# Kernel optimization log

Measured on AMD Instinct MI355X. Metric: run time of the kernel, lower is better.

Reference implementation:

```python
import jax, jax.numpy as jnp
import numpy as np

B, N, D, W = 4, 4096, 256, 7
K = 2 * W + 1  # 15 taps: positions [i-2w, ..., i]
H = 4 * D
EPS = 1e-5


def layer_norm(x, g, b):
    mu = jnp.mean(x, axis=-1, keepdims=True)
    var = jnp.mean(jnp.square(x - mu), axis=-1, keepdims=True)
    return (x - mu) * jax.lax.rsqrt(var + EPS) * g + b


def setup_inputs() -> dict:
    key = jax.random.key(0)
    ks = jax.random.split(key, 8)
    s = 0.02
    return {
        "x": jax.random.normal(ks[0], (B, N, D), dtype=jnp.float32),
        # w_mix[k] is the DxD block of the (K*D -> D) Linear acting on offset k-2w
        "w_mix": (jax.random.normal(ks[1], (K, D, D), dtype=jnp.float32) * s),
        "b_mix": jnp.zeros((D,), dtype=jnp.float32),
        "g1": jnp.ones((D,), jnp.float32) + 0.1 * jax.random.normal(ks[2], (D,), jnp.float32),
        "b1": 0.1 * jax.random.normal(ks[3], (D,), jnp.float32),
        "w_ff1": jax.random.normal(ks[4], (D, H), dtype=jnp.float32) * s,
        "b_ff1": jnp.zeros((H,), dtype=jnp.float32),
        "w_ff2": jax.random.normal(ks[5], (H, D), dtype=jnp.float32) * s,
        "b_ff2": jnp.zeros((D,), dtype=jnp.float32),
        "g2": jnp.ones((D,), jnp.float32) + 0.1 * jax.random.normal(ks[6], (D,), jnp.float32),
        "b2": 0.1 * jax.random.normal(ks[7], (D,), jnp.float32),
    }


def reference(x, w_mix, b_mix, g1, b1, w_ff1, b_ff1, w_ff2, b_ff2, g2, b2):
    # Causal windowed concat + Linear == causal 1D conv with kernel K=2w+1.
    # torch feats chunk k holds x[i - 2w + k]; conv tap k with left pad 2w
    # sees exactly x[i - 2w + k], so kernel = mix weight reshaped (K, D, D).
    mix = jax.lax.conv_general_dilated(
        x, w_mix, window_strides=(1,), padding=[(2 * W, 0)],
        dimension_numbers=("NWC", "WIO", "NWC"),
    ) + b_mix  # [B, N, D]
    # Dropout is identity in eval mode (reference baseline).
    h = layer_norm(x + mix, g1, b1)
    ff = jnp.dot(jax.nn.gelu(jnp.dot(h, w_ff1) + b_ff1, approximate=False), w_ff2) + b_ff2
    return layer_norm(h + ff, g2, b2)
```

## Files before the change

kernel.cpp:

```cpp
#include <hip/hip_runtime.h>
#include <cstdint>

#define DD     256
#define HH     1024
#define NNSEQ  4096
#define MT     32
#define XR     46
#define XPITCH 264
#define SLOTP  260
#define EPSLN  1e-5f

typedef unsigned short u16;
typedef __attribute__((ext_vector_type(8))) short short8;
typedef __attribute__((ext_vector_type(4))) float f32x4;

#define MFMA(a, b, c) __builtin_amdgcn_mfma_f32_16x16x32_bf16(a, b, c, 0, 0, 0)

__device__ __forceinline__ u16 f2bf(float f) {
  unsigned u = __float_as_uint(f);
  u += 0x7FFF + ((u >> 16) & 1);
  return (u16)(u >> 16);
}
__device__ __forceinline__ float bf2f(u16 s) { return __uint_as_float(((unsigned)s) << 16); }

__device__ __forceinline__ float fast_gelu(float v) {
  const float e = __expf(v * __builtin_fmaf(v * v, -0.0713548163f, -1.5957691216f));
  return v * __builtin_amdgcn_rcpf(1.f + e);
}

__global__ __launch_bounds__(256) void k_prep(
    const float* __restrict__ wmix, const float* __restrict__ wff1,
    const float* __restrict__ wff2, u16* __restrict__ wpk,
    u16* __restrict__ w1pk, u16* __restrict__ w2pk)
{
  __shared__ float t[32][257];
  const int b = blockIdx.x, tid = threadIdx.x;

  u16* dst;
  if (b < 120) {
    dst = wpk + (size_t)b * 8192;
    for (int r = 0; r < 32; ++r)
      t[r][tid] = wmix[(size_t)(b * 32 + r) * 256 + tid];
  } else if (b < 152) {
    const int u = b - 120, c2 = u >> 3, s = u & 7;
    dst = w1pk + (size_t)u * 8192;
    for (int r = 0; r < 32; ++r)
      t[r][tid] = wff1[(size_t)(s * 32 + r) * 1024 + c2 * 256 + tid];
  } else {
    const int u = b - 152, c2 = u >> 3, s = u & 7;
    dst = w2pk + (size_t)u * 8192;
    for (int r = 0; r < 32; ++r)
      t[r][tid] = wff2[(size_t)(c2 * 256 + s * 32 + r) * 256 + tid];
  }
  __syncthreads();

  const int l = tid & 63, q = l >> 4, cl = l & 15;
#pragma unroll
  for (int f = 0; f < 4; ++f) {
    const int fi = f * 4 + (tid >> 6);
    const int n = fi * 16 + cl;
    uint4 pk;
    unsigned* p = (unsigned*)&pk;
#pragma unroll
    for (int jj = 0; jj < 4; ++jj)
      p[jj] = (unsigned)f2bf(t[q * 8 + jj * 2][n]) | ((unsigned)f2bf(t[q * 8 + jj * 2 + 1][n]) << 16);
    *(uint4*)&dst[(size_t)fi * 512 + l * 8] = pk;
  }
}

__global__ __launch_bounds__(512, 4) void k_fused(
    const float* __restrict__ x, const u16* __restrict__ wpk,
    const float* __restrict__ bmix, const float* __restrict__ g1,
    const float* __restrict__ b1, const u16* __restrict__ w1pk,
    const float* __restrict__ bf1, const u16* __restrict__ w2pk,
    const float* __restrict__ bf2, const float* __restrict__ g2,
    const float* __restrict__ b2, float* __restrict__ out)
{
  __shared__ __align__(16) u16 bufA[XR * XPITCH];
  __shared__ __align__(16) u16 asbuf[2 * MT * XPITCH];
  __shared__ float redS[8][MT], redS2[8][MT];
  __shared__ float muL[MT], invL[MT];

#define bufB ((float*)asbuf)

  const int tid = threadIdx.x;
  const int wv = tid >> 6, l = tid & 63, q = l >> 4, cl = l & 15;
  const int mg = wv >> 2, ng = wv & 3;
  const long tok0 = (long)blockIdx.x * MT;
  const int n0 = (int)(tok0 & (NNSEQ - 1));

  {
    const int cslot = (tid & 63) * 4;
    for (int r = tid >> 6; r < XR; r += 8) {
      const int nloc = n0 - 14 + r;
      float4 v = make_float4(0.f, 0.f, 0.f, 0.f);
      if (nloc >= 0) v = *(const float4*)&x[(tok0 - 14 + r) * DD + cslot];
      uint2 pk;
      pk.x = (unsigned)f2bf(v.x) | ((unsigned)f2bf(v.y) << 16);
      pk.y = (unsigned)f2bf(v.z) | ((unsigned)f2bf(v.w) << 16);
      *(uint2*)&bufA[r * XPITCH + cslot] = pk;
    }
  }
  __syncthreads();

  f32x4 acc[2][4];
#pragma unroll
  for (int nt = 0; nt < 4; ++nt) {
    const float bm = (mg == 0) ? bmix[ng * 64 + nt * 16 + cl] : 0.f;
#pragma unroll
    for (int mt = 0; mt < 2; ++mt) acc[mt][nt] = (f32x4){bm, bm, bm, bm};
  }

  const u16* bbase = wpk + (size_t)(mg * 60) * 8192 + (size_t)(ng * 4) * 512 + (size_t)l * 8;

#define LOAD_A(dst, s_)                                                         \
  {                                                                             \
    const int ks = mg * 60 + (s_);                                              \
    const int xrow = ks >> 3, c0 = (ks & 7) * 32;                               \
    _Pragma("unroll")                                                           \
    for (int mt = 0; mt < 2; ++mt)                                              \
      dst[mt] = *(const short8*)&bufA[(xrow + mt * 16 + cl) * XPITCH + c0 + q * 8]; \
  }
#define LOAD_B(dst, s_)                                                         \
  {                                                                             \
    const u16* bp = bbase + (size_t)(s_) * 8192;                                \
    _Pragma("unroll")                                                           \
    for (int nt = 0; nt < 4; ++nt)                                              \
      dst[nt] = *(const short8*)(bp + nt * 512);                                \
  }

  {
    short8 af[2][2], bfr[2][4];
    LOAD_A(af[0], 0) LOAD_B(bfr[0], 0)
    LOAD_A(af[1], 1) LOAD_B(bfr[1], 1)

#pragma unroll 2
    for (int s = 0; s < 60; ++s) {
      const int cur = s & 1;
#pragma unroll
      for (int mt = 0; mt < 2; ++mt)
#pragma unroll
        for (int nt = 0; nt < 4; ++nt)
          acc[mt][nt] = MFMA(af[cur][mt], bfr[cur][nt], acc[mt][nt]);
      if (s + 2 < 60) {
        LOAD_A(af[cur], s + 2)
        LOAD_B(bfr[cur], s + 2)
      }
    }
  }
#undef LOAD_A
#undef LOAD_B

  if (mg == 1) {
#pragma unroll
    for (int mt = 0; mt < 2; ++mt)
#pragma unroll
      for (int nt = 0; nt < 4; ++nt)
#pragma unroll
        for (int reg = 0; reg < 4; ++reg)
          bufB[(mt * 16 + q * 4 + reg) * SLOTP + ng * 64 + nt * 16 + cl] = acc[mt][nt][reg];
  }
  __syncthreads();

  if (mg == 0) {
    float ps[2][4], ps2[2][4];
#pragma unroll
    for (int mt = 0; mt < 2; ++mt)
#pragma unroll
      for (int reg = 0; reg < 4; ++reg) {
        const int row = mt * 16 + q * 4 + reg;
        float s = 0.f, s2 = 0.f;
#pragma unroll
        for (int nt = 0; nt < 4; ++nt) {
          const int col = ng * 64 + nt * 16 + cl;
          const float y = acc[mt][nt][reg] + bufB[row * SLOTP + col]
                        + x[(tok0 + row) * DD + col];
          acc[mt][nt][reg] = y;
          s += y; s2 += y * y;
        }
#pragma unroll
        for (int off = 1; off < 16; off <<= 1) { s += __shfl_xor(s, off, 64); s2 += __shfl_xor(s2, off, 64); }
        ps[mt][reg] = s; ps2[mt][reg] = s2;
      }
    if (cl == 0) {
#pragma unroll
      for (int mt = 0; mt < 2; ++mt)
#pragma unroll
        for (int reg = 0; reg < 4; ++reg) {
          const int row = mt * 16 + q * 4 + reg;
          redS[ng][row] = ps[mt][reg]; redS2[ng][row] = ps2[mt][reg];
        }
    }
  }
  __syncthreads();
  if (tid < MT) {
    const float s  = redS[0][tid] + redS[1][tid] + redS[2][tid] + redS[3][tid];
    const float s2 = redS2[0][tid] + redS2[1][tid] + redS2[2][tid] + redS2[3][tid];
    const float mu = s * (1.f / DD);
    const float var = s2 * (1.f / DD) - mu * mu;
    muL[tid] = mu; invL[tid] = rsqrtf(var + EPSLN);
  }
  __syncthreads();

  if (mg == 0) {
#pragma unroll
    for (int nt = 0; nt < 4; ++nt) {
      const int col = ng * 64 + nt * 16 + cl;
      const float gv = g1[col], bv = b1[col];
#pragma unroll
      for (int mt = 0; mt < 2; ++mt)
#pragma unroll
        for (int reg = 0; reg < 4; ++reg) {
          const int row = mt * 16 + q * 4 + reg;
          const float hv = (acc[mt][nt][reg] - muL[row]) * invL[row] * gv + bv;
          bufA[row * XPITCH + col] = f2bf(hv);
        }
    }
  }
  __syncthreads();

  f32x4 acc2[2][2];
#pragma unroll
  for (int nt = 0; nt < 2; ++nt) {
    const float bv = bf2[wv * 32 + nt * 16 + cl];
#pragma unroll
    for (int mt = 0; mt < 2; ++mt) acc2[mt][nt] = (f32x4){bv, bv, bv, bv};
  }

  for (int c = 0; c < 4; ++c) {
    u16* asb = asbuf + (c & 1) * (MT * XPITCH);
    f32x4 acc1[2][2];
#pragma unroll
    for (int nt = 0; nt < 2; ++nt) {
      const float bv = bf1[c * 256 + wv * 32 + nt * 16 + cl];
#pragma unroll
      for (int mt = 0; mt < 2; ++mt) acc1[mt][nt] = (f32x4){bv, bv, bv, bv};
    }
#pragma unroll 2
    for (int s = 0; s < 8; ++s) {
      short8 a[2], b[2];
#pragma unroll
      for (int mt = 0; mt < 2; ++mt)
        a[mt] = *(const short8*)&bufA[(mt * 16 + cl) * XPITCH + s * 32 + q * 8];
      const u16* bp = w1pk + (size_t)(c * 8 + s) * 8192 + (size_t)(wv * 2) * 512 + (size_t)l * 8;
#pragma unroll
      for (int nt = 0; nt < 2; ++nt)
        b[nt] = *(const short8*)(bp + nt * 512);
#pragma unroll
      for (int mt = 0; mt < 2; ++mt)
#pragma unroll
        for (int nt = 0; nt < 2; ++nt)
          acc1[mt][nt] = MFMA(a[mt], b[nt], acc1[mt][nt]);
    }
#pragma unroll
    for (int mt = 0; mt < 2; ++mt)
#pragma unroll
      for (int nt = 0; nt < 2; ++nt)
#pragma unroll
        for (int reg = 0; reg < 4; ++reg) {
          const float g = fast_gelu(acc1[mt][nt][reg]);
          asb[(mt * 16 + q * 4 + reg) * XPITCH + wv * 32 + nt * 16 + cl] = f2bf(g);
        }
    __syncthreads();
#pragma unroll 2
    for (int s = 0; s < 8; ++s) {
      short8 a[2], b[2];
#pragma unroll
      for (int mt = 0; mt < 2; ++mt)
        a[mt] = *(const short8*)&asb[(mt * 16 + cl) * XPITCH + s * 32 + q * 8];
      const u16* bp = w2pk + (size_t)(c * 8 + s) * 8192 + (size_t)(wv * 2) * 512 + (size_t)l * 8;
#pragma unroll
      for (int nt = 0; nt < 2; ++nt)
        b[nt] = *(const short8*)(bp + nt * 512);
#pragma unroll
      for (int mt = 0; mt < 2; ++mt)
#pragma unroll
        for (int nt = 0; nt < 2; ++nt)
          acc2[mt][nt] = MFMA(a[mt], b[nt], acc2[mt][nt]);
    }
  }

  {
    float ps[2][4], ps2[2][4];
#pragma unroll
    for (int mt = 0; mt < 2; ++mt)
#pragma unroll
      for (int reg = 0; reg < 4; ++reg) {
        const int row = mt * 16 + q * 4 + reg;
        float s = 0.f, s2 = 0.f;
#pragma unroll
        for (int nt = 0; nt < 2; ++nt) {
          const int col = wv * 32 + nt * 16 + cl;
          const float y = acc2[mt][nt][reg] + bf2f(bufA[row * XPITCH + col]);
          acc2[mt][nt][reg] = y;
          s += y; s2 += y * y;
        }
#pragma unroll
        for (int off = 1; off < 16; off <<= 1) { s += __shfl_xor(s, off, 64); s2 += __shfl_xor(s2, off, 64); }
        ps[mt][reg] = s; ps2[mt][reg] = s2;
      }
    if (cl == 0) {
#pragma unroll
      for (int mt = 0; mt < 2; ++mt)
#pragma unroll
        for (int reg = 0; reg < 4; ++reg) {
          const int row = mt * 16 + q * 4 + reg;
          redS[wv][row] = ps[mt][reg]; redS2[wv][row] = ps2[mt][reg];
        }
    }
  }
  __syncthreads();
  if (tid < MT) {
    float s = 0.f, s2 = 0.f;
#pragma unroll
    for (int k = 0; k < 8; ++k) { s += redS[k][tid]; s2 += redS2[k][tid]; }
    const float mu = s * (1.f / DD);
    const float var = s2 * (1.f / DD) - mu * mu;
    muL[tid] = mu; invL[tid] = rsqrtf(var + EPSLN);
  }
  __syncthreads();

#pragma unroll
  for (int nt = 0; nt < 2; ++nt) {
    const int col = wv * 32 + nt * 16 + cl;
    const float gv = g2[col], bv = b2[col];
#pragma unroll
    for (int mt = 0; mt < 2; ++mt)
#pragma unroll
      for (int reg = 0; reg < 4; ++reg) {
        const int row = mt * 16 + q * 4 + reg;
        out[(tok0 + row) * DD + col] = (acc2[mt][nt][reg] - muL[row]) * invL[row] * gv + bv;
      }
  }
#undef bufB
}

extern "C" void kernel_launch(void* const* d_in, const int* in_sizes, int n_in,
                              void* d_out, int out_size, void* d_ws, size_t ws_size,
                              hipStream_t stream) {
  const float* x    = (const float*)d_in[0];
  const float* wmix = (const float*)d_in[1];
  const float* bmix = (const float*)d_in[2];
  const float* g1   = (const float*)d_in[3];
  const float* b1   = (const float*)d_in[4];
  const float* wff1 = (const float*)d_in[5];
  const float* bff1 = (const float*)d_in[6];
  const float* wff2 = (const float*)d_in[7];
  const float* bff2 = (const float*)d_in[8];
  const float* g2   = (const float*)d_in[9];
  const float* b2   = (const float*)d_in[10];
  float* out = (float*)d_out;

  u16* wpk  = (u16*)d_ws;
  u16* w1pk = wpk + 983040;
  u16* w2pk = w1pk + 262144;

  k_prep<<<184, 256, 0, stream>>>(wmix, wff1, wff2, wpk, w1pk, w2pk);

  k_fused<<<512, 512, 0, stream>>>(x, wpk, bmix, g1, b1,
                                   w1pk, bff1, w2pk, bff2, g2, b2, out);
}
```

Before: 155.0 us.

## Split conv GEMM by output columns across all waves, halve LDS buffers

```diff
diff --git a/kernel.cpp b/kernel.cpp
--- a/kernel.cpp
+++ b/kernel.cpp
@@ -7,7 +7,6 @@
 #define MT     32
 #define XR     46
 #define XPITCH 264
-#define SLOTP  260
 #define EPSLN  1e-5f
 
 typedef unsigned short u16;
@@ -68,7 +67,7 @@
   }
 }
 
-__global__ __launch_bounds__(512, 4) void k_fused(
+__global__ __launch_bounds__(512, 6) void k_fused(
     const float* __restrict__ x, const u16* __restrict__ wpk,
     const float* __restrict__ bmix, const float* __restrict__ g1,
     const float* __restrict__ b1, const u16* __restrict__ w1pk,
@@ -77,21 +76,18 @@
     const float* __restrict__ b2, float* __restrict__ out)
 {
   __shared__ __align__(16) u16 bufA[XR * XPITCH];
-  __shared__ __align__(16) u16 asbuf[2 * MT * XPITCH];
+  __shared__ __align__(16) u16 asb[MT * XPITCH];
   __shared__ float redS[8][MT], redS2[8][MT];
   __shared__ float muL[MT], invL[MT];
 
-#define bufB ((float*)asbuf)
-
   const int tid = threadIdx.x;
   const int wv = tid >> 6, l = tid & 63, q = l >> 4, cl = l & 15;
-  const int mg = wv >> 2, ng = wv & 3;
   const long tok0 = (long)blockIdx.x * MT;
   const int n0 = (int)(tok0 & (NNSEQ - 1));
 
   {
-    const int cslot = (tid & 63) * 4;
-    for (int r = tid >> 6; r < XR; r += 8) {
+    const int cslot = l * 4;
+    for (int r = wv; r < XR; r += 8) {
       const int nloc = n0 - 14 + r;
       float4 v = make_float4(0.f, 0.f, 0.f, 0.f);
       if (nloc >= 0) v = *(const float4*)&x[(tok0 - 14 + r) * DD + cslot];
@@ -103,20 +99,19 @@
   }
   __syncthreads();
 
-  f32x4 acc[2][4];
-#pragma unroll
-  for (int nt = 0; nt < 4; ++nt) {
-    const float bm = (mg == 0) ? bmix[ng * 64 + nt * 16 + cl] : 0.f;
+  f32x4 acc[2][2];
+#pragma unroll
+  for (int nt = 0; nt < 2; ++nt) {
+    const float bm = bmix[wv * 32 + nt * 16 + cl];
 #pragma unroll
     for (int mt = 0; mt < 2; ++mt) acc[mt][nt] = (f32x4){bm, bm, bm, bm};
   }
 
-  const u16* bbase = wpk + (size_t)(mg * 60) * 8192 + (size_t)(ng * 4) * 512 + (size_t)l * 8;
+  const u16* bbase = wpk + (size_t)(wv * 2) * 512 + (size_t)l * 8;
 
 #define LOAD_A(dst, s_)                                                         \
   {                                                                             \
-    const int ks = mg * 60 + (s_);                                              \
-    const int xrow = ks >> 3, c0 = (ks & 7) * 32;                               \
+    const int xrow = (s_) >> 3, c0 = ((s_) & 7) * 32;                           \
     _Pragma("unroll")                                                           \
     for (int mt = 0; mt < 2; ++mt)                                              \
       dst[mt] = *(const short8*)&bufA[(xrow + mt * 16 + cl) * XPITCH + c0 + q * 8]; \
@@ -125,24 +120,24 @@
   {                                                                             \
     const u16* bp = bbase + (size_t)(s_) * 8192;                                \
     _Pragma("unroll")                                                           \
-    for (int nt = 0; nt < 4; ++nt)                                              \
+    for (int nt = 0; nt < 2; ++nt)                                              \
       dst[nt] = *(const short8*)(bp + nt * 512);                                \
   }
 
   {
-    short8 af[2][2], bfr[2][4];
+    short8 af[2][2], bfr[2][2];
     LOAD_A(af[0], 0) LOAD_B(bfr[0], 0)
     LOAD_A(af[1], 1) LOAD_B(bfr[1], 1)
 
 #pragma unroll 2
-    for (int s = 0; s < 60; ++s) {
+    for (int s = 0; s < 120; ++s) {
       const int cur = s & 1;
 #pragma unroll
       for (int mt = 0; mt < 2; ++mt)
 #pragma unroll
-        for (int nt = 0; nt < 4; ++nt)
+        for (int nt = 0; nt < 2; ++nt)
           acc[mt][nt] = MFMA(af[cur][mt], bfr[cur][nt], acc[mt][nt]);
-      if (s + 2 < 60) {
+      if (s + 2 < 120) {
         LOAD_A(af[cur], s + 2)
         LOAD_B(bfr[cur], s + 2)
       }
@@ -151,18 +146,7 @@
 #undef LOAD_A
 #undef LOAD_B
 
-  if (mg == 1) {
-#pragma unroll
-    for (int mt = 0; mt < 2; ++mt)
-#pragma unroll
-      for (int nt = 0; nt < 4; ++nt)
-#pragma unroll
-        for (int reg = 0; reg < 4; ++reg)
-          bufB[(mt * 16 + q * 4 + reg) * SLOTP + ng * 64 + nt * 16 + cl] = acc[mt][nt][reg];
-  }
-  __syncthreads();
-
-  if (mg == 0) {
+  {
     float ps[2][4], ps2[2][4];
 #pragma unroll
     for (int mt = 0; mt < 2; ++mt)
@@ -171,10 +155,9 @@
         const int row = mt * 16 + q * 4 + reg;
         float s = 0.f, s2 = 0.f;
 #pragma unroll
-        for (int nt = 0; nt < 4; ++nt) {
-          const int col = ng * 64 + nt * 16 + cl;
-          const float y = acc[mt][nt][reg] + bufB[row * SLOTP + col]
-                        + x[(tok0 + row) * DD + col];
+        for (int nt = 0; nt < 2; ++nt) {
+          const int col = wv * 32 + nt * 16 + cl;
+          const float y = acc[mt][nt][reg] + x[(tok0 + row) * DD + col];
           acc[mt][nt][reg] = y;
           s += y; s2 += y * y;
         }
@@ -188,34 +171,33 @@
 #pragma unroll
         for (int reg = 0; reg < 4; ++reg) {
           const int row = mt * 16 + q * 4 + reg;
-          redS[ng][row] = ps[mt][reg]; redS2[ng][row] = ps2[mt][reg];
+          redS[wv][row] = ps[mt][reg]; redS2[wv][row] = ps2[mt][reg];
         }
     }
   }
   __syncthreads();
   if (tid < MT) {
-    const float s  = redS[0][tid] + redS[1][tid] + redS[2][tid] + redS[3][tid];
-    const float s2 = redS2[0][tid] + redS2[1][tid] + redS2[2][tid] + redS2[3][tid];
+    float s = 0.f, s2 = 0.f;
+#pragma unroll
+    for (int k = 0; k < 8; ++k) { s += redS[k][tid]; s2 += redS2[k][tid]; }
     const float mu = s * (1.f / DD);
     const float var = s2 * (1.f / DD) - mu * mu;
     muL[tid] = mu; invL[tid] = rsqrtf(var + EPSLN);
   }
   __syncthreads();
 
-  if (mg == 0) {
-#pragma unroll
-    for (int nt = 0; nt < 4; ++nt) {
-      const int col = ng * 64 + nt * 16 + cl;
-      const float gv = g1[col], bv = b1[col];
-#pragma unroll
-      for (int mt = 0; mt < 2; ++mt)
-#pragma unroll
-        for (int reg = 0; reg < 4; ++reg) {
-          const int row = mt * 16 + q * 4 + reg;
-          const float hv = (acc[mt][nt][reg] - muL[row]) * invL[row] * gv + bv;
-          bufA[row * XPITCH + col] = f2bf(hv);
-        }
-    }
+#pragma unroll
+  for (int nt = 0; nt < 2; ++nt) {
+    const int col = wv * 32 + nt * 16 + cl;
+    const float gv = g1[col], bv = b1[col];
+#pragma unroll
+    for (int mt = 0; mt < 2; ++mt)
+#pragma unroll
+      for (int reg = 0; reg < 4; ++reg) {
+        const int row = mt * 16 + q * 4 + reg;
+        const float hv = (acc[mt][nt][reg] - muL[row]) * invL[row] * gv + bv;
+        bufA[row * XPITCH + col] = f2bf(hv);
+      }
   }
   __syncthreads();
 
@@ -228,7 +210,6 @@
   }
 
   for (int c = 0; c < 4; ++c) {
-    u16* asb = asbuf + (c & 1) * (MT * XPITCH);
     f32x4 acc1[2][2];
 #pragma unroll
     for (int nt = 0; nt < 2; ++nt) {
@@ -278,6 +259,7 @@
         for (int nt = 0; nt < 2; ++nt)
           acc2[mt][nt] = MFMA(a[mt], b[nt], acc2[mt][nt]);
     }
+    __syncthreads();
   }
 
   {
@@ -332,7 +314,6 @@
         out[(tok0 + row) * DD + col] = (acc2[mt][nt][reg] - muL[row]) * invL[row] * gv + bv;
       }
   }
-#undef bufB
 }
 
 extern "C" void kernel_launch(void* const* d_in, const int* in_sizes, int n_in,
```

New measurement: 161.7 us. 1.04x slower.

## Deepen register prefetch pipeline for conv and FFN MFMA loops

Applied to the files above, without the earlier changes.

```diff
diff --git a/kernel.cpp b/kernel.cpp
--- a/kernel.cpp
+++ b/kernel.cpp
@@ -89,9 +89,18 @@
   const long tok0 = (long)blockIdx.x * MT;
   const int n0 = (int)(tok0 & (NNSEQ - 1));
 
+  f32x4 acc[2][4];
+#pragma unroll
+  for (int nt = 0; nt < 4; ++nt) {
+    const float bm = (mg == 0) ? bmix[ng * 64 + nt * 16 + cl] : 0.f;
+#pragma unroll
+    for (int mt = 0; mt < 2; ++mt) acc[mt][nt] = (f32x4){bm, bm, bm, bm};
+  }
+  const u16* bbase = wpk + (size_t)(mg * 60) * 8192 + (size_t)(ng * 4) * 512 + (size_t)l * 8;
+
   {
-    const int cslot = (tid & 63) * 4;
-    for (int r = tid >> 6; r < XR; r += 8) {
+    const int cslot = l * 4;
+    for (int r = wv; r < XR; r += 8) {
       const int nloc = n0 - 14 + r;
       float4 v = make_float4(0.f, 0.f, 0.f, 0.f);
       if (nloc >= 0) v = *(const float4*)&x[(tok0 - 14 + r) * DD + cslot];
@@ -101,17 +110,6 @@
       *(uint2*)&bufA[r * XPITCH + cslot] = pk;
     }
   }
-  __syncthreads();
-
-  f32x4 acc[2][4];
-#pragma unroll
-  for (int nt = 0; nt < 4; ++nt) {
-    const float bm = (mg == 0) ? bmix[ng * 64 + nt * 16 + cl] : 0.f;
-#pragma unroll
-    for (int mt = 0; mt < 2; ++mt) acc[mt][nt] = (f32x4){bm, bm, bm, bm};
-  }
-
-  const u16* bbase = wpk + (size_t)(mg * 60) * 8192 + (size_t)(ng * 4) * 512 + (size_t)l * 8;
 
 #define LOAD_A(dst, s_)                                                         \
   {                                                                             \
@@ -130,22 +128,34 @@
   }
 
   {
-    short8 af[2][2], bfr[2][4];
-    LOAD_A(af[0], 0) LOAD_B(bfr[0], 0)
-    LOAD_A(af[1], 1) LOAD_B(bfr[1], 1)
-
-#pragma unroll 2
-    for (int s = 0; s < 60; ++s) {
-      const int cur = s & 1;
+    short8 af[3][2], bfr[3][4];
+    LOAD_B(bfr[0], 0)
+    LOAD_B(bfr[1], 1)
+    LOAD_B(bfr[2], 2)
+    __syncthreads();
+    LOAD_A(af[0], 0)
+    LOAD_A(af[1], 1)
+    LOAD_A(af[2], 2)
+
+    for (int sb = 0; sb < 57; sb += 3) {
+#pragma unroll
+      for (int u = 0; u < 3; ++u) {
+#pragma unroll
+        for (int mt = 0; mt < 2; ++mt)
+#pragma unroll
+          for (int nt = 0; nt < 4; ++nt)
+            acc[mt][nt] = MFMA(af[u][mt], bfr[u][nt], acc[mt][nt]);
+        LOAD_A(af[u], sb + u + 3)
+        LOAD_B(bfr[u], sb + u + 3)
+      }
+    }
+#pragma unroll
+    for (int u = 0; u < 3; ++u) {
 #pragma unroll
       for (int mt = 0; mt < 2; ++mt)
 #pragma unroll
         for (int nt = 0; nt < 4; ++nt)
-          acc[mt][nt] = MFMA(af[cur][mt], bfr[cur][nt], acc[mt][nt]);
-      if (s + 2 < 60) {
-        LOAD_A(af[cur], s + 2)
-        LOAD_B(bfr[cur], s + 2)
-      }
+          acc[mt][nt] = MFMA(af[u][mt], bfr[u][nt], acc[mt][nt]);
     }
   }
 #undef LOAD_A
@@ -227,6 +237,20 @@
     for (int mt = 0; mt < 2; ++mt) acc2[mt][nt] = (f32x4){bv, bv, bv, bv};
   }
 
+#define FF_LDA(src, dst, s_)                                                    \
+  {                                                                             \
+    _Pragma("unroll")                                                           \
+    for (int mt = 0; mt < 2; ++mt)                                              \
+      dst[mt] = *(const short8*)&src[(mt * 16 + cl) * XPITCH + (s_) * 32 + q * 8]; \
+  }
+#define FF_LDB(wsrc, dst, s_)                                                   \
+  {                                                                             \
+    const u16* bp = wsrc + (size_t)(c * 8 + (s_)) * 8192 + (size_t)(wv * 2) * 512 + (size_t)l * 8; \
+    _Pragma("unroll")                                                           \
+    for (int nt = 0; nt < 2; ++nt)                                              \
+      dst[nt] = *(const short8*)(bp + nt * 512);                                \
+  }
+
   for (int c = 0; c < 4; ++c) {
     u16* asb = asbuf + (c & 1) * (MT * XPITCH);
     f32x4 acc1[2][2];
@@ -236,21 +260,29 @@
 #pragma unroll
       for (int mt = 0; mt < 2; ++mt) acc1[mt][nt] = (f32x4){bv, bv, bv, bv};
     }
-#pragma unroll 2
-    for (int s = 0; s < 8; ++s) {
-      short8 a[2], b[2];
-#pragma unroll
-      for (int mt = 0; mt < 2; ++mt)
-        a[mt] = *(const short8*)&bufA[(mt * 16 + cl) * XPITCH + s * 32 + q * 8];
-      const u16* bp = w1pk + (size_t)(c * 8 + s) * 8192 + (size_t)(wv * 2) * 512 + (size_t)l * 8;
-#pragma unroll
-      for (int nt = 0; nt < 2; ++nt)
-        b[nt] = *(const short8*)(bp + nt * 512);
-#pragma unroll
-      for (int mt = 0; mt < 2; ++mt)
-#pragma unroll
-        for (int nt = 0; nt < 2; ++nt)
-          acc1[mt][nt] = MFMA(a[mt], b[nt], acc1[mt][nt]);
+    {
+      short8 a2[2][2], b2r[2][2];
+      FF_LDA(bufA, a2[0], 0) FF_LDB(w1pk, b2r[0], 0)
+      FF_LDA(bufA, a2[1], 1) FF_LDB(w1pk, b2r[1], 1)
+#pragma unroll
+      for (int s = 0; s < 6; ++s) {
+        const int cur = s & 1;
+#pragma unroll
+        for (int mt = 0; mt < 2; ++mt)
+#pragma unroll
+          for (int nt = 0; nt < 2; ++nt)
+            acc1[mt][nt] = MFMA(a2[cur][mt], b2r[cur][nt], acc1[mt][nt]);
+        FF_LDA(bufA, a2[cur], s + 2) FF_LDB(w1pk, b2r[cur], s + 2)
+      }
+#pragma unroll
+      for (int s = 6; s < 8; ++s) {
+        const int cur = s & 1;
+#pragma unroll
+        for (int mt = 0; mt < 2; ++mt)
+#pragma unroll
+          for (int nt = 0; nt < 2; ++nt)
+            acc1[mt][nt] = MFMA(a2[cur][mt], b2r[cur][nt], acc1[mt][nt]);
+      }
     }
 #pragma unroll
     for (int mt = 0; mt < 2; ++mt)
@@ -262,23 +294,33 @@
           asb[(mt * 16 + q * 4 + reg) * XPITCH + wv * 32 + nt * 16 + cl] = f2bf(g);
         }
     __syncthreads();
-#pragma unroll 2
-    for (int s = 0; s < 8; ++s) {
-      short8 a[2], b[2];
-#pragma unroll
-      for (int mt = 0; mt < 2; ++mt)
-        a[mt] = *(const short8*)&asb[(mt * 16 + cl) * XPITCH + s * 32 + q * 8];
-      const u16* bp = w2pk + (size_t)(c * 8 + s) * 8192 + (size_t)(wv * 2) * 512 + (size_t)l * 8;
-#pragma unroll
-      for (int nt = 0; nt < 2; ++nt)
-        b[nt] = *(const short8*)(bp + nt * 512);
-#pragma unroll
-      for (int mt = 0; mt < 2; ++mt)
-#pragma unroll
-        for (int nt = 0; nt < 2; ++nt)
-          acc2[mt][nt] = MFMA(a[mt], b[nt], acc2[mt][nt]);
-    }
-  }
+    {
+      short8 a2[2][2], b2r[2][2];
+      FF_LDA(asb, a2[0], 0) FF_LDB(w2pk, b2r[0], 0)
+      FF_LDA(asb, a2[1], 1) FF_LDB(w2pk, b2r[1], 1)
+#pragma unroll
+      for (int s = 0; s < 6; ++s) {
+        const int cur = s & 1;
+#pragma unroll
+        for (int mt = 0; mt < 2; ++mt)
+#pragma unroll
+          for (int nt = 0; nt < 2; ++nt)
+            acc2[mt][nt] = MFMA(a2[cur][mt], b2r[cur][nt], acc2[mt][nt]);
+        FF_LDA(asb, a2[cur], s + 2) FF_LDB(w2pk, b2r[cur], s + 2)
+      }
+#pragma unroll
+      for (int s = 6; s < 8; ++s) {
+        const int cur = s & 1;
+#pragma unroll
+        for (int mt = 0; mt < 2; ++mt)
+#pragma unroll
+          for (int nt = 0; nt < 2; ++nt)
+            acc2[mt][nt] = MFMA(a2[cur][mt], b2r[cur][nt], acc2[mt][nt]);
+      }
+    }
+  }
+#undef FF_LDA
+#undef FF_LDB
 
   {
     float ps[2][4], ps2[2][4];
```

Result: no change. 154.8 us (-0.1%).
